# Kernel optimization log

Hardware: AMD Instinct MI355X
Metric: run time of the kernel (lower is better)

Reference implementation:

```python
import jax, jax.numpy as jnp
import numpy as np

N = 16777216  # rows
G = 1024      # distinct group keys (power of 2 -> no binary-search padding)


def setup_inputs() -> dict:
    key = jax.random.key(0)
    k1, k2, k3 = jax.random.split(key, 3)
    # guarantee every group id in [0, G) appears at least once
    base = jnp.arange(G, dtype=jnp.int32)
    rest = jax.random.randint(k1, (N - G,), 0, G, dtype=jnp.int32)
    key_col = jax.random.permutation(k2, jnp.concatenate([base, rest])).reshape(-1, 1)
    val_col = jax.random.normal(k3, (N, 1), dtype=jnp.float32)
    return {"key_col": key_col, "val_col": val_col}


def _group_indices(x_flat, uniq_desc):
    # Faithful vectorized replication of find_mapping_indices: binary search of each
    # x against the reverse-sorted (descending) unique keys. G is a power of 2 so
    # N_prime == G and no front padding occurs.
    steps = int(np.log2(G))
    offset = G // 2
    pos = (x_flat <= uniq_desc[offset]).astype(jnp.int32) * offset
    offset = offset // 2  # int(ceil(offset/2)) == offset//2 for powers of two
    for _ in range(1, steps):
        bins = (x_flat <= uniq_desc[pos + offset]).astype(jnp.int32)
        pos = pos + bins * offset
        offset = offset // 2
    return pos  # [N] group index in [0, G)


def reference(key_col, val_col):
    x = key_col.reshape(-1)
    v = val_col.reshape(-1)
    # torch.sort(torch.unique(x), descending=True): all G values present by construction
    uniq_desc = jnp.unique(x, size=G)[::-1]
    gid = _group_indices(x, uniq_desc)
    # fused segmented reduces replace the per-group masked_select loop (same math)
    s = jax.ops.segment_sum(v, gid, num_segments=G)
    cnt = jax.ops.segment_sum(jnp.ones_like(v), gid, num_segments=G)
    avg = s / cnt  # torch.mean per group; every group non-empty
    mn = jax.ops.segment_min(v, gid, num_segments=G)
    mx = jax.ops.segment_max(v, gid, num_segments=G)
    # group_selection_mask is all-True (every group occupied) -> masked_select is identity
    key_out = uniq_desc.reshape(-1, 1)
    return (key_out,
            s.reshape(-1, 1),
            avg.reshape(-1, 1),
            mn.reshape(-1, 1),
            mx.reshape(-1, 1))
```

## Files before the change

### kernel.cpp

```cpp
#include <hip/hip_runtime.h>

#define G 1024
#define SCALEF 1048576.0f
#define CNT_SHIFT 42
#define ELEM_BIAS (1 << 24)
#define LOW_MASK ((1ULL << CNT_SHIFT) - 1)
#define NREP 8

__device__ __forceinline__ unsigned omap(float x) {
    unsigned u = __float_as_uint(x);
    return (u & 0x80000000u) ? ~u : (u | 0x80000000u);
}
__device__ __forceinline__ float ounmap(unsigned o) {
    unsigned u = (o & 0x80000000u) ? (o & 0x7fffffffu) : ~o;
    return __uint_as_float(u);
}

__global__ __launch_bounds__(256) void gb_warm(
    const int4* __restrict__ keys, const float4* __restrict__ vals, int n4w,
    unsigned long long* __restrict__ rsum, unsigned* __restrict__ rcnt,
    unsigned* __restrict__ rmaxo, unsigned* __restrict__ rminv)
{
    __shared__ unsigned long long s_sc[G];
    __shared__ uint2              s_mm[G];
    for (int k = threadIdx.x; k < G; k += 256) {
        s_sc[k] = 0ull;
        s_mm[k] = make_uint2(0xffffffffu, 0u);
    }
    __syncthreads();

    const int stride = gridDim.x * 256;
    for (int i = blockIdx.x * 256 + threadIdx.x; i < n4w; i += stride) {
        int4 k4 = keys[i]; float4 v4 = vals[i];
#define WARM_ELEM(KK, VV)                                                      \
        {                                                                      \
            const int k = (KK); const float v = (VV);                          \
            const unsigned o = omap(v);                                        \
            uint2 mm = s_mm[k];                                                \
            if (o < mm.x) atomicMin(&s_mm[k].x, o);                            \
            if (o > mm.y) atomicMax(&s_mm[k].y, o);                            \
            const int vf = __float2int_rn(v * SCALEF);                         \
            atomicAdd(&s_sc[k], (1ULL << CNT_SHIFT) +                          \
                      (unsigned long long)(unsigned)(vf + ELEM_BIAS));         \
        }
        WARM_ELEM(k4.x, v4.x) WARM_ELEM(k4.y, v4.y)
        WARM_ELEM(k4.z, v4.z) WARM_ELEM(k4.w, v4.w)
#undef WARM_ELEM
    }
    __syncthreads();

    const int r = blockIdx.x & (NREP - 1);
    for (int k = threadIdx.x; k < G; k += 256) {
        const unsigned long long cell = s_sc[k];
        const unsigned n = (unsigned)(cell >> CNT_SHIFT);
        if (n) {
            const long long sfx = (long long)(cell & LOW_MASK) - ((long long)n << 24);
            const uint2 mm = s_mm[k];
            atomicAdd(&rsum[r * G + k], (unsigned long long)sfx);
            atomicAdd(&rcnt[r * G + k], n);
            atomicMax(&rmaxo[r * G + k], mm.y);
            atomicMax(&rminv[r * G + k], ~mm.x);
        }
    }
}

__global__ __launch_bounds__(256) void gb_gate(
    const unsigned* __restrict__ rmaxo, const unsigned* __restrict__ rminv,
    unsigned* __restrict__ gate)
{
    const int k = blockIdx.x * 256 + threadIdx.x;
    unsigned mx = 0u, mv = 0u;
    for (int r = 0; r < NREP; ++r) {
        mx = max(mx, rmaxo[r * G + k]);
        mv = max(mv, rminv[r * G + k]);
    }
    const unsigned min_o = ~mv;
    gate[k] = (min_o & 0xffff0000u) | (mx >> 16);
}

__global__ __launch_bounds__(256) void gb_main(
    const int4* __restrict__ keys, const float4* __restrict__ vals,
    int i0, int n4,
    unsigned long long* __restrict__ rsum, unsigned* __restrict__ rcnt,
    unsigned* __restrict__ rmaxo, unsigned* __restrict__ rminv,
    const unsigned* __restrict__ gate)
{
    __shared__ unsigned long long s_sc[G];
    __shared__ unsigned           s_gate[G];
    for (int k = threadIdx.x; k < G; k += 256) {
        s_sc[k]   = 0ull;
        s_gate[k] = gate[k];
    }
    __syncthreads();

    const int r = blockIdx.x & (NREP - 1);
    unsigned* __restrict__ rmaxo_r = rmaxo + r * G;
    unsigned* __restrict__ rminv_r = rminv + r * G;

#define MAIN_ELEM(KK, VV)                                                      \
        {                                                                      \
            const int k = (KK); const float v = (VV);                          \
            const unsigned o  = omap(v);                                       \
            const unsigned g  = s_gate[k];                                     \
            const unsigned ot = o >> 16;                                       \
            if (ot <= (g >> 16))     atomicMax(&rminv_r[k], ~o);               \
            if (ot >= (g & 0xffffu)) atomicMax(&rmaxo_r[k], o);                \
            const int vf = __float2int_rn(v * SCALEF);                         \
            atomicAdd(&s_sc[k], (1ULL << CNT_SHIFT) +                          \
                      (unsigned long long)(unsigned)(vf + ELEM_BIAS));         \
        }

    const int stride = gridDim.x * 256;
    int i = i0 + blockIdx.x * 256 + threadIdx.x;
    if (i < n4) {
        int4 k4 = keys[i]; float4 v4 = vals[i];
        for (i += stride; ; i += stride) {
            const bool more = (i < n4);
            int4 nk; float4 nv;
            if (more) { nk = keys[i]; nv = vals[i]; }
            MAIN_ELEM(k4.x, v4.x) MAIN_ELEM(k4.y, v4.y)
            MAIN_ELEM(k4.z, v4.z) MAIN_ELEM(k4.w, v4.w)
            if (!more) break;
            k4 = nk; v4 = nv;
        }
    }
#undef MAIN_ELEM
    __syncthreads();

    for (int k = threadIdx.x; k < G; k += 256) {
        const unsigned long long cell = s_sc[k];
        const unsigned n = (unsigned)(cell >> CNT_SHIFT);
        if (n) {
            const long long sfx = (long long)(cell & LOW_MASK) - ((long long)n << 24);
            atomicAdd(&rsum[r * G + k], (unsigned long long)sfx);
            atomicAdd(&rcnt[r * G + k], n);
        }
    }
}

__global__ __launch_bounds__(256) void gb_write(
    const unsigned long long* __restrict__ rsum, const unsigned* __restrict__ rcnt,
    const unsigned* __restrict__ rmaxo, const unsigned* __restrict__ rminv,
    float* __restrict__ out)
{
    const int k = blockIdx.x * 256 + threadIdx.x;
    long long ts = 0ll; unsigned tc = 0u, mx = 0u, mv = 0u;
    for (int r = 0; r < NREP; ++r) {
        ts += (long long)rsum[r * G + k];
        tc += rcnt[r * G + k];
        mx = max(mx, rmaxo[r * G + k]);
        mv = max(mv, rminv[r * G + k]);
    }
    const float sum = (float)((double)ts * (1.0 / (double)SCALEF));
    const int g = (G - 1) - k;
    out[g]         = (float)k;
    out[G + g]     = sum;
    out[2 * G + g] = sum / (float)tc;
    out[3 * G + g] = ounmap(~mv);
    out[4 * G + g] = ounmap(mx);
}

extern "C" void kernel_launch(void* const* d_in, const int* in_sizes, int n_in,
                              void* d_out, int out_size, void* d_ws, size_t ws_size,
                              hipStream_t stream) {
    const int4*   keys = (const int4*)d_in[0];
    const float4* vals = (const float4*)d_in[1];
    const int n   = in_sizes[0];
    const int n4  = n / 4;
    int n4w = n4 >> 4;
    if (n4w < 1)  n4w = (n4 < 1) ? 0 : n4;
    if (n4w > n4) n4w = n4;

    unsigned long long* rsum  = (unsigned long long*)d_ws;
    unsigned*           rcnt  = (unsigned*)(rsum + NREP * G);
    unsigned*           rmaxo = rcnt + NREP * G;
    unsigned*           rminv = rmaxo + NREP * G;
    unsigned*           gate  = rminv + NREP * G;
    const size_t acc_bytes = (size_t)NREP * G * (8 + 4 + 4 + 4);

    hipMemsetAsync(d_ws, 0, acc_bytes, stream);

    hipLaunchKernelGGL(gb_warm, dim3(256), dim3(256), 0, stream,
                       keys, vals, n4w, rsum, rcnt, rmaxo, rminv);
    hipLaunchKernelGGL(gb_gate, dim3(G / 256), dim3(256), 0, stream,
                       rmaxo, rminv, gate);
    hipLaunchKernelGGL(gb_main, dim3(2048), dim3(256), 0, stream,
                       keys, vals, n4w, n4, rsum, rcnt, rmaxo, rminv, gate);
    hipLaunchKernelGGL(gb_write, dim3(G / 256), dim3(256), 0, stream,
                       rsum, rcnt, rmaxo, rminv, (float*)d_out);
}
```

Measured before the change: 172.4 us.

## Replace per-group min/max gates with global thresholds and pack sum+count atomics

The per-group 16-bit gate table in shared memory is replaced by two global thresholds: the maximum of all per-group warm-up minima and the minimum of all per-group warm-up maxima, reduced in a single-block gate kernel. The main loop now compares the full 32-bit ordered value against these scalars instead of loading a per-key gate from shared memory. Separately, sum and count are packed into one 64-bit global atomic per group, halving the flush atomics. Global thresholds are looser than per-group ones, so more elements may pass the filter and issue global min/max atomics. The packed layout also limits the headroom of the fixed-point sum field.

```diff
diff --git a/kernel.cpp b/kernel.cpp
--- a/kernel.cpp
+++ b/kernel.cpp
@@ -5,6 +5,8 @@
 #define CNT_SHIFT 42
 #define ELEM_BIAS (1 << 24)
 #define LOW_MASK ((1ULL << CNT_SHIFT) - 1)
+#define GCNT_SHIFT 44
+#define GLOW_MASK ((1ULL << GCNT_SHIFT) - 1)
 #define NREP 8
 
 __device__ __forceinline__ unsigned omap(float x) {
@@ -16,9 +18,14 @@
     return __uint_as_float(u);
 }
 
+__device__ __forceinline__ unsigned long long pack_gcell(unsigned n, long long s) {
+    return ((unsigned long long)n << GCNT_SHIFT) +
+           (unsigned long long)(s + ((long long)n << 23));
+}
+
 __global__ __launch_bounds__(256) void gb_warm(
     const int4* __restrict__ keys, const float4* __restrict__ vals, int n4w,
-    unsigned long long* __restrict__ rsum, unsigned* __restrict__ rcnt,
+    unsigned long long* __restrict__ racc,
     unsigned* __restrict__ rmaxo, unsigned* __restrict__ rminv)
 {
     __shared__ unsigned long long s_sc[G];
@@ -54,43 +61,52 @@
         const unsigned long long cell = s_sc[k];
         const unsigned n = (unsigned)(cell >> CNT_SHIFT);
         if (n) {
-            const long long sfx = (long long)(cell & LOW_MASK) - ((long long)n << 24);
+            const long long s = (long long)(cell & LOW_MASK) - ((long long)n << 24);
             const uint2 mm = s_mm[k];
-            atomicAdd(&rsum[r * G + k], (unsigned long long)sfx);
-            atomicAdd(&rcnt[r * G + k], n);
+            atomicAdd(&racc[r * G + k], pack_gcell(n, s));
             atomicMax(&rmaxo[r * G + k], mm.y);
             atomicMax(&rminv[r * G + k], ~mm.x);
         }
     }
 }
 
-__global__ __launch_bounds__(256) void gb_gate(
+__global__ __launch_bounds__(1024) void gb_gate(
     const unsigned* __restrict__ rmaxo, const unsigned* __restrict__ rminv,
-    unsigned* __restrict__ gate)
-{
-    const int k = blockIdx.x * 256 + threadIdx.x;
+    unsigned* __restrict__ gate2)
+{
+    const int k = threadIdx.x;
     unsigned mx = 0u, mv = 0u;
     for (int r = 0; r < NREP; ++r) {
         mx = max(mx, rmaxo[r * G + k]);
         mv = max(mv, rminv[r * G + k]);
     }
-    const unsigned min_o = ~mv;
-    gate[k] = (min_o & 0xffff0000u) | (mx >> 16);
+    __shared__ unsigned l_tmin[1024];
+    __shared__ unsigned l_tmax[1024];
+    l_tmin[k] = ~mv;
+    l_tmax[k] = mx;
+    __syncthreads();
+    for (int s = 512; s > 0; s >>= 1) {
+        if (k < s) {
+            l_tmin[k] = max(l_tmin[k], l_tmin[k + s]);
+            l_tmax[k] = min(l_tmax[k], l_tmax[k + s]);
+        }
+        __syncthreads();
+    }
+    if (k == 0) { gate2[0] = l_tmin[0]; gate2[1] = l_tmax[0]; }
 }
 
 __global__ __launch_bounds__(256) void gb_main(
     const int4* __restrict__ keys, const float4* __restrict__ vals,
     int i0, int n4,
-    unsigned long long* __restrict__ rsum, unsigned* __restrict__ rcnt,
+    unsigned long long* __restrict__ racc,
     unsigned* __restrict__ rmaxo, unsigned* __restrict__ rminv,
-    const unsigned* __restrict__ gate)
+    const unsigned* __restrict__ gate2)
 {
     __shared__ unsigned long long s_sc[G];
-    __shared__ unsigned           s_gate[G];
-    for (int k = threadIdx.x; k < G; k += 256) {
-        s_sc[k]   = 0ull;
-        s_gate[k] = gate[k];
-    }
+    for (int k = threadIdx.x; k < G; k += 256) s_sc[k] = 0ull;
+
+    const unsigned Tmin = gate2[0];
+    const unsigned Tmax = gate2[1];
     __syncthreads();
 
     const int r = blockIdx.x & (NREP - 1);
@@ -100,11 +116,9 @@
 #define MAIN_ELEM(KK, VV)                                                      \
         {                                                                      \
             const int k = (KK); const float v = (VV);                          \
-            const unsigned o  = omap(v);                                       \
-            const unsigned g  = s_gate[k];                                     \
-            const unsigned ot = o >> 16;                                       \
-            if (ot <= (g >> 16))     atomicMax(&rminv_r[k], ~o);               \
-            if (ot >= (g & 0xffffu)) atomicMax(&rmaxo_r[k], o);                \
+            const unsigned o = omap(v);                                        \
+            if (o <= Tmin) atomicMax(&rminv_r[k], ~o);                         \
+            if (o >= Tmax) atomicMax(&rmaxo_r[k], o);                          \
             const int vf = __float2int_rn(v * SCALEF);                         \
             atomicAdd(&s_sc[k], (1ULL << CNT_SHIFT) +                          \
                       (unsigned long long)(unsigned)(vf + ELEM_BIAS));         \
@@ -131,31 +145,31 @@
         const unsigned long long cell = s_sc[k];
         const unsigned n = (unsigned)(cell >> CNT_SHIFT);
         if (n) {
-            const long long sfx = (long long)(cell & LOW_MASK) - ((long long)n << 24);
-            atomicAdd(&rsum[r * G + k], (unsigned long long)sfx);
-            atomicAdd(&rcnt[r * G + k], n);
+            const long long s = (long long)(cell & LOW_MASK) - ((long long)n << 24);
+            atomicAdd(&racc[r * G + k], pack_gcell(n, s));
         }
     }
 }
 
 __global__ __launch_bounds__(256) void gb_write(
-    const unsigned long long* __restrict__ rsum, const unsigned* __restrict__ rcnt,
+    const unsigned long long* __restrict__ racc,
     const unsigned* __restrict__ rmaxo, const unsigned* __restrict__ rminv,
     float* __restrict__ out)
 {
     const int k = blockIdx.x * 256 + threadIdx.x;
-    long long ts = 0ll; unsigned tc = 0u, mx = 0u, mv = 0u;
+    unsigned long long cell = 0ull; unsigned mx = 0u, mv = 0u;
     for (int r = 0; r < NREP; ++r) {
-        ts += (long long)rsum[r * G + k];
-        tc += rcnt[r * G + k];
+        cell += racc[r * G + k];
         mx = max(mx, rmaxo[r * G + k]);
         mv = max(mv, rminv[r * G + k]);
     }
-    const float sum = (float)((double)ts * (1.0 / (double)SCALEF));
+    const unsigned n = (unsigned)(cell >> GCNT_SHIFT);
+    const long long s = (long long)(cell & GLOW_MASK) - ((long long)n << 23);
+    const float sum = (float)((double)s * (1.0 / (double)SCALEF));
     const int g = (G - 1) - k;
     out[g]         = (float)k;
     out[G + g]     = sum;
-    out[2 * G + g] = sum / (float)tc;
+    out[2 * G + g] = sum / (float)n;
     out[3 * G + g] = ounmap(~mv);
     out[4 * G + g] = ounmap(mx);
 }
@@ -171,21 +185,20 @@
     if (n4w < 1)  n4w = (n4 < 1) ? 0 : n4;
     if (n4w > n4) n4w = n4;
 
-    unsigned long long* rsum  = (unsigned long long*)d_ws;
-    unsigned*           rcnt  = (unsigned*)(rsum + NREP * G);
-    unsigned*           rmaxo = rcnt + NREP * G;
+    unsigned long long* racc  = (unsigned long long*)d_ws;
+    unsigned*           rmaxo = (unsigned*)(racc + NREP * G);
     unsigned*           rminv = rmaxo + NREP * G;
-    unsigned*           gate  = rminv + NREP * G;
-    const size_t acc_bytes = (size_t)NREP * G * (8 + 4 + 4 + 4);
+    unsigned*           gate2 = rminv + NREP * G;
+    const size_t acc_bytes = (size_t)NREP * G * (8 + 4 + 4) + 2 * sizeof(unsigned);
 
     hipMemsetAsync(d_ws, 0, acc_bytes, stream);
 
     hipLaunchKernelGGL(gb_warm, dim3(256), dim3(256), 0, stream,
-                       keys, vals, n4w, rsum, rcnt, rmaxo, rminv);
-    hipLaunchKernelGGL(gb_gate, dim3(G / 256), dim3(256), 0, stream,
-                       rmaxo, rminv, gate);
+                       keys, vals, n4w, racc, rmaxo, rminv);
+    hipLaunchKernelGGL(gb_gate, dim3(1), dim3(1024), 0, stream,
+                       rmaxo, rminv, gate2);
     hipLaunchKernelGGL(gb_main, dim3(2048), dim3(256), 0, stream,
-                       keys, vals, n4w, n4, rsum, rcnt, rmaxo, rminv, gate);
+                       keys, vals, n4w, n4, racc, rmaxo, rminv, gate2);
     hipLaunchKernelGGL(gb_write, dim3(G / 256), dim3(256), 0, stream,
-                       rsum, rcnt, rmaxo, rminv, (float*)d_out);
-}
+                       racc, rmaxo, rminv, (float*)d_out);
+}
```

Result: faster. 168.9 us (-2.0%).
